# Kernel optimization log

Hardware: AMD Instinct MI355X
Metric: run time of the kernel (lower is better)

The kernel has to match this reference:

```python
import jax, jax.numpy as jnp
import numpy as np

P = 16          # patch size
ER = 2          # expand_ratio = per-head dim in Hgru2

def _shift2d(x, sh, sw):
    # zero-fill shift of (B,C,H,W) image by (sh, sw); matches torch F.pad((l,r,t,b)) with a negative crop
    H, W = x.shape[2], x.shape[3]
    ah, aw = abs(sh), abs(sw)
    xp = jnp.pad(x, ((0, 0), (0, 0), (ah, ah), (aw, aw)))
    return xp[:, :, ah - sh:ah - sh + H, aw - sw:aw - sw + W]

def _layernorm(x, g, b, eps=1e-5):
    m = jnp.mean(x, axis=-1, keepdims=True)
    v = jnp.var(x, axis=-1, keepdims=True)
    return (x - m) * jax.lax.rsqrt(v + eps) * g + b

def _rmsnorm(x, eps=1e-6):
    # FastSimpleRMSNorm: weightless RMS normalization
    return x * jax.lax.rsqrt(jnp.mean(x * x, axis=-1, keepdims=True) + eps)

def _hgru2(x, lb_vec, wi, wo):
    # x: (N, T, D). NOTE: the torch module unpacks x.shape as (n, b, d), so the
    # gated linear recurrence scans over axis 0 exactly as the original does.
    N, T, D = x.shape
    H = D // ER
    feat = x @ wi                                    # (N, T, 3D)
    V, Q, Fg = jnp.split(feat, 3, axis=-1)
    V = jax.nn.gelu(V, approximate=False).reshape(N, T, H, ER)
    Q = jax.nn.gelu(Q, approximate=False).reshape(N, T, H, ER)
    Fg = jax.nn.sigmoid(Fg).reshape(N, T, H, ER)
    lb = lb_vec.reshape(H, ER)
    lam = lb + (1.0 - lb) * Fg                       # decay lambda_t in (lb, 1)
    K = 1.0 - lam
    def step(S, inp):
        q, k, v, l = inp                             # each (T, H, ER)
        # S[t,h,i,j] = lam[i] * S + k[i] * v[j]  (GLA recurrence, 2x2 state/head)
        S = l[..., None] * S + k[..., None] * v[..., None, :]
        o = jnp.einsum('thi,thij->thj', q, S)
        return S, o
    S0 = jnp.zeros((T, H, ER, ER), dtype=x.dtype)
    _, o = jax.lax.scan(step, S0, (Q, K, V, lam))    # o: (N, T, H, ER)
    return o.reshape(N, T, D) @ wo

def reference(img, spt_ln_g, spt_ln_b, spt_w, spt_b, pos_emb, cls_token, lower_bounds,
              in_proj_w, out_proj_w, ff_w1, ff_b1, ff_w2, ff_b2,
              head_ln_g, head_ln_b, head_w, head_b):
    B, C, Hh, Ww = img.shape
    # SPT: concat original + 4 shifted copies on channel axis -> (B, 5C, H, W)
    xs = jnp.concatenate([img,
                          _shift2d(img, 0, 1), _shift2d(img, 0, -1),
                          _shift2d(img, 1, 0), _shift2d(img, -1, 0)], axis=1)
    c5 = 5 * C
    h, w = Hh // P, Ww // P
    # 'b c (h p1) (w p2) -> b (h w) (p1 p2 c)'
    patches = xs.reshape(B, c5, h, P, w, P).transpose(0, 2, 4, 3, 5, 1).reshape(B, h * w, P * P * c5)
    tokens = _layernorm(patches, spt_ln_g, spt_ln_b) @ spt_w + spt_b   # (B, NP, D)
    n = tokens.shape[1]
    cls = jnp.broadcast_to(cls_token, (B, 1, tokens.shape[2]))
    x = jnp.concatenate([cls, tokens], axis=1) + pos_emb[:, :n + 1]
    # layer-wise monotone lower bounds for the decay gate
    lb = jax.nn.softmax(lower_bounds, axis=0)
    lb = jnp.cumsum(lb, axis=0)
    lb = lb - lb[0]
    depth = lower_bounds.shape[0]
    for i in range(depth):
        x = _hgru2(_rmsnorm(x), lb[i], in_proj_w[i], out_proj_w[i]) + x
        hmid = jax.nn.gelu(_rmsnorm(x) @ ff_w1[i] + ff_b1[i], approximate=False)
        x = hmid @ ff_w2[i] + ff_b2[i] + x
    x = _rmsnorm(x)
    x = x[:, 0]                                      # cls pooling
    return _layernorm(x, head_ln_g, head_ln_b) @ head_w + head_b

def setup_inputs():
    key = jax.random.key(0)
    ks = jax.random.split(key, 10)
    B, C, IMG, D, DEPTH, MLP, NC = 16, 3, 256, 768, 8, 3072, 1000
    NP = (IMG // P) ** 2
    PD = P * P * 5 * C
    s = 0.02
    return {
        'img': jax.random.normal(ks[0], (B, C, IMG, IMG), jnp.float32),
        'spt_ln_g': jnp.ones((PD,), jnp.float32),
        'spt_ln_b': jnp.zeros((PD,), jnp.float32),
        'spt_w': jax.random.normal(ks[1], (PD, D), jnp.float32) * s,
        'spt_b': jnp.zeros((D,), jnp.float32),
        'pos_emb': jax.random.normal(ks[2], (1, NP + 1, D), jnp.float32),
        'cls_token': jax.random.normal(ks[3], (1, 1, D), jnp.float32),
        'lower_bounds': jnp.ones((DEPTH, D), jnp.float32),
        'in_proj_w': jax.random.normal(ks[4], (DEPTH, D, 3 * D), jnp.float32) * s,
        'out_proj_w': jax.random.normal(ks[5], (DEPTH, D, D), jnp.float32) * s,
        'ff_w1': jax.random.normal(ks[6], (DEPTH, D, MLP), jnp.float32) * s,
        'ff_b1': jnp.zeros((DEPTH, MLP), jnp.float32),
        'ff_w2': jax.random.normal(ks[7], (DEPTH, MLP, D), jnp.float32) * s,
        'ff_b2': jnp.zeros((DEPTH, D), jnp.float32),
        'head_ln_g': jnp.ones((D,), jnp.float32),
        'head_ln_b': jnp.zeros((D,), jnp.float32),
        'head_w': jax.random.normal(ks[8], (D, NC), jnp.float32) * s,
        'head_b': jnp.zeros((NC,), jnp.float32),
    }
```

## Files before the change

### kernel.cpp

```cpp
#include <hip/hip_runtime.h>
#include <hip/hip_bf16.h>

typedef __bf16 bf16x8 __attribute__((ext_vector_type(8)));
typedef float floatx4 __attribute__((ext_vector_type(4)));

#define DEV __device__ __forceinline__

DEV float gelu_f(float x) {
    return 0.5f * x * (1.0f + erff(x * 0.70710678118654752f));
}

DEV void block_reduce2(float& a, float& b, float* s) {
    #pragma unroll
    for (int o = 32; o > 0; o >>= 1) {
        a += __shfl_down(a, o, 64);
        b += __shfl_down(b, o, 64);
    }
    __syncthreads();
    int wv = threadIdx.x >> 6;
    if ((threadIdx.x & 63) == 0) { s[wv * 2] = a; s[wv * 2 + 1] = b; }
    __syncthreads();
    int nw = blockDim.x >> 6;
    float ra = 0.f, rb = 0.f;
    for (int i = 0; i < nw; ++i) { ra += s[i * 2]; rb += s[i * 2 + 1]; }
    a = ra; b = rb;
}

__global__ __launch_bounds__(256) void compute_lb(const float* __restrict__ lbin, float* __restrict__ lbout) {
    int d = blockIdx.x * 256 + threadIdx.x;
    if (d >= 768) return;
    float v[8];
    float mx = -1e30f;
    #pragma unroll
    for (int i = 0; i < 8; ++i) { v[i] = lbin[i * 768 + d]; mx = fmaxf(mx, v[i]); }
    float s = 0.f;
    #pragma unroll
    for (int i = 0; i < 8; ++i) { v[i] = expf(v[i] - mx); s += v[i]; }
    float inv = 1.f / s;
    float first = v[0] * inv;
    float cum = 0.f;
    #pragma unroll
    for (int i = 0; i < 8; ++i) { cum += v[i] * inv; lbout[i * 768 + d] = cum - first; }
}

__global__ __launch_bounds__(256) void init_tokens(const float* __restrict__ cls, const float* __restrict__ pos,
                                                   const float* __restrict__ bias, float* __restrict__ x) {
    int i = blockIdx.x * 256 + threadIdx.x;
    if (i >= 16 * 257 * 768) return;
    int d = i % 768;
    int row = i / 768;
    int t = row % 257;
    float v;
    if (t == 0) v = cls[d] + pos[d];
    else        v = bias[d] + pos[(size_t)t * 768 + d];
    x[(size_t)row * 768 + d] = v;
}

__global__ __launch_bounds__(256) void patch_ln(const float* __restrict__ img, const float* __restrict__ g,
                                                const float* __restrict__ bt, __hip_bfloat16* __restrict__ out) {
    int pm = blockIdx.x;
    int b = pm >> 8, pp = pm & 255;
    int ph = pp >> 4, pw = pp & 15;
    __shared__ float pv[3840];
    __shared__ float sbuf[8];
    float s = 0.f, ss = 0.f;
    #pragma unroll
    for (int i = 0; i < 15; ++i) {
        int f = threadIdx.x + i * 256;
        int pi = f / 15, cc = f % 15;
        int ip = pi >> 4, jp = pi & 15;
        int g5 = cc / 3, ch = cc % 3;
        int sh = (g5 == 3) - (g5 == 4);
        int sw = (g5 == 1) - (g5 == 2);
        int y = ph * 16 + ip - sh;
        int x = pw * 16 + jp - sw;
        float val = 0.f;
        if ((unsigned)y < 256u && (unsigned)x < 256u)
            val = img[(((size_t)b * 3 + ch) * 256 + y) * 256 + x];
        pv[f] = val; s += val; ss += val * val;
    }
    block_reduce2(s, ss, sbuf);
    float mean = s * (1.f / 3840.f);
    float var  = ss * (1.f / 3840.f) - mean * mean;
    float inv  = rsqrtf(var + 1e-5f);
    #pragma unroll
    for (int i = 0; i < 15; ++i) {
        int f = threadIdx.x + i * 256;
        out[(size_t)pm * 3840 + f] = __float2bfloat16((pv[f] - mean) * inv * g[f] + bt[f]);
    }
}

__global__ __launch_bounds__(256) void transpose_cast(const float* __restrict__ W, __hip_bfloat16* __restrict__ Wt,
                                                      int K, int N) {
    __shared__ float tile[32][33];
    int k0 = blockIdx.x * 32, n0 = blockIdx.y * 32;
    int tx = threadIdx.x & 31, ty = threadIdx.x >> 5;
    #pragma unroll
    for (int i = 0; i < 4; ++i) {
        int k = ty + i * 8;
        tile[k][tx] = W[(size_t)(k0 + k) * N + n0 + tx];
    }
    __syncthreads();
    #pragma unroll
    for (int i = 0; i < 4; ++i) {
        int n = ty + i * 8;
        Wt[(size_t)(n0 + n) * K + k0 + tx] = __float2bfloat16(tile[tx][n]);
    }
}

__global__ __launch_bounds__(256) void rmsnorm_kernel(const float* __restrict__ x, __hip_bfloat16* __restrict__ out) {
    int row = blockIdx.x;
    const float* xr = x + (size_t)row * 768;
    __shared__ float sbuf[8];
    float v[3];
    float ss = 0.f, d0 = 0.f;
    #pragma unroll
    for (int i = 0; i < 3; ++i) { v[i] = xr[threadIdx.x + i * 256]; ss += v[i] * v[i]; }
    block_reduce2(ss, d0, sbuf);
    float scale = rsqrtf(ss * (1.f / 768.f) + 1e-6f);
    #pragma unroll
    for (int i = 0; i < 3; ++i)
        out[(size_t)row * 768 + threadIdx.x + i * 256] = __float2bfloat16(v[i] * scale);
}

__global__ __launch_bounds__(256) void hgru_scan(const float* __restrict__ feat, __hip_bfloat16* __restrict__ o) {
    int idx = blockIdx.x * 256 + threadIdx.x;
    if (idx >= 257 * 384) return;
    int t = idx / 384, h = idx % 384;
    float2 V[16], Q[16], L[16];
    #pragma unroll
    for (int n = 0; n < 16; ++n) {
        size_t base = ((size_t)n * 257 + t) * 2304 + h * 2;
        V[n] = *(const float2*)(feat + base);
        Q[n] = *(const float2*)(feat + base + 768);
        L[n] = *(const float2*)(feat + base + 1536);
    }
    float S00 = 0.f, S01 = 0.f, S10 = 0.f, S11 = 0.f;
    #pragma unroll
    for (int n = 0; n < 16; ++n) {
        float l0 = L[n].x, l1 = L[n].y;
        float k0 = 1.f - l0, k1 = 1.f - l1;
        S00 = l0 * S00 + k0 * V[n].x; S01 = l0 * S01 + k0 * V[n].y;
        S10 = l1 * S10 + k1 * V[n].x; S11 = l1 * S11 + k1 * V[n].y;
        float o0 = Q[n].x * S00 + Q[n].y * S10;
        float o1 = Q[n].x * S01 + Q[n].y * S11;
        __hip_bfloat162 ov;
        ov.x = __float2bfloat16(o0);
        ov.y = __float2bfloat16(o1);
        *(__hip_bfloat162*)(o + ((size_t)n * 257 + t) * 768 + h * 2) = ov;
    }
}

__global__ __launch_bounds__(256) void head_kernel(const float* __restrict__ x, const float* __restrict__ g,
                                                   const float* __restrict__ be, const float* __restrict__ hw,
                                                   const float* __restrict__ hb, float* __restrict__ out) {
    int b = blockIdx.x;
    const float* xr = x + (size_t)b * 257 * 768;
    __shared__ float z[768];
    __shared__ float sbuf[8];
    float v[3];
    float ss = 0.f, d0 = 0.f;
    #pragma unroll
    for (int i = 0; i < 3; ++i) { v[i] = xr[threadIdx.x + i * 256]; ss += v[i] * v[i]; }
    block_reduce2(ss, d0, sbuf);
    float rs = rsqrtf(ss * (1.f / 768.f) + 1e-6f);
    float s = 0.f, s2 = 0.f;
    #pragma unroll
    for (int i = 0; i < 3; ++i) { float y = v[i] * rs; s += y; s2 += y * y; }
    block_reduce2(s, s2, sbuf);
    float mean = s * (1.f / 768.f);
    float var  = s2 * (1.f / 768.f) - mean * mean;
    float inv  = rsqrtf(var + 1e-5f);
    #pragma unroll
    for (int i = 0; i < 3; ++i) {
        int d = threadIdx.x + i * 256;
        z[d] = (v[i] * rs - mean) * inv * g[d] + be[d];
    }
    __syncthreads();
    int j = blockIdx.y * 256 + threadIdx.x;
    if (j < 1000) {
        float acc = hb[j];
        for (int d = 0; d < 768; ++d) acc += z[d] * hw[d * 1000 + j];
        out[b * 1000 + j] = acc;
    }
}

template<int EPI, int BN, int DEPTH>
__global__ __launch_bounds__(256) void gemm_bt(
        const __hip_bfloat16* __restrict__ A, const __hip_bfloat16* __restrict__ Bt,
        int N, int Ktot, int Mvalid,
        float* __restrict__ outf, __hip_bfloat16* __restrict__ outb,
        const float* __restrict__ bias, const float* __restrict__ aux) {
    constexpr int WNF = BN / 32;
    __shared__ alignas(16) __hip_bfloat16 Als[DEPTH][128 * 32];
    __shared__ alignas(16) __hip_bfloat16 Bls[DEPTH][BN * 32];
    const int tid  = threadIdx.x;
    const int lane = tid & 63;
    const int wv   = tid >> 6;

    const int gx = gridDim.x;
    const int nwg = gx * gridDim.y;
    const int orig = blockIdx.x + gx * blockIdx.y;
    const int q = nwg >> 3, r = nwg & 7;
    const int xcd = orig & 7, off = orig >> 3;
    const int wg = (xcd < r ? xcd * (q + 1) : r * (q + 1) + (xcd - r) * q) + off;
    const int n0 = (wg % gx) * BN;
    const int m0 = (wg / gx) * 128;

    const int wm = wv & 1, wn = wv >> 1;
    const int fr = lane & 15;
    const int fq = lane >> 4;
    const int srow = lane >> 2;
    const int ssw  = (((lane & 3) ^ ((srow >> 1) & 3)) * 8);
    const int rsw  = ((fq ^ ((fr >> 1) & 3)) * 8);

    floatx4 acc[4][WNF];
    #pragma unroll
    for (int mi = 0; mi < 4; ++mi)
        #pragma unroll
        for (int ni = 0; ni < WNF; ++ni)
            acc[mi][ni] = (floatx4){0.f, 0.f, 0.f, 0.f};

    auto stage = [&](int kt, int buf) {
        #pragma unroll
        for (int j = 0; j < 2; ++j) {
            int cc = wv * 2 + j;
            const __hip_bfloat16* ga = A + (size_t)(m0 + cc * 16 + srow) * Ktot + kt + ssw;
            __builtin_amdgcn_global_load_lds((const __attribute__((address_space(1))) void*)ga,
                                             (__attribute__((address_space(3))) void*)(&Als[buf][cc * 512]), 16, 0, 0);
        }
        #pragma unroll
        for (int j = 0; j < BN / 64; ++j) {
            int cc = wv * (BN / 64) + j;
            const __hip_bfloat16* gb = Bt + (size_t)(n0 + cc * 16 + srow) * Ktot + kt + ssw;
            __builtin_amdgcn_global_load_lds((const __attribute__((address_space(1))) void*)gb,
                                             (__attribute__((address_space(3))) void*)(&Bls[buf][cc * 512]), 16, 0, 0);
        }
    };

    const int nk = Ktot / 32;
    #pragma unroll
    for (int t = 0; t < DEPTH - 1; ++t) stage(t * 32, t);

    int cur = 0;
    for (int i = 0; i < nk; ++i) {
        if constexpr (DEPTH == 4) {
            if (i + 2 < nk)      asm volatile("s_waitcnt vmcnt(6)" ::: "memory");
            else if (i + 1 < nk) asm volatile("s_waitcnt vmcnt(3)" ::: "memory");
            else                 asm volatile("s_waitcnt vmcnt(0)" ::: "memory");
        } else {
            if (i + 1 < nk) {
                if constexpr (BN == 128) asm volatile("s_waitcnt vmcnt(4)" ::: "memory");
                else                     asm volatile("s_waitcnt vmcnt(3)" ::: "memory");
            } else {
                asm volatile("s_waitcnt vmcnt(0)" ::: "memory");
            }
        }
        __builtin_amdgcn_s_barrier();
        __builtin_amdgcn_sched_barrier(0);

        bf16x8 af[4], bfv[WNF];
        #pragma unroll
        for (int mi = 0; mi < 4; ++mi)
            af[mi] = *(const bf16x8*)((const void*)&Als[cur][(wm * 64 + mi * 16 + fr) * 32 + rsw]);
        #pragma unroll
        for (int ni = 0; ni < WNF; ++ni)
            bfv[ni] = *(const bf16x8*)((const void*)&Bls[cur][(wn * (BN / 2) + ni * 16 + fr) * 32 + rsw]);

        if (i + DEPTH - 1 < nk) stage((i + DEPTH - 1) * 32, cur == 0 ? DEPTH - 1 : cur - 1);

        #pragma unroll
        for (int mi = 0; mi < 4; ++mi)
            #pragma unroll
            for (int ni = 0; ni < WNF; ++ni)
                acc[mi][ni] = __builtin_amdgcn_mfma_f32_16x16x32_bf16(af[mi], bfv[ni], acc[mi][ni], 0, 0, 0);

        cur = (cur == DEPTH - 1) ? 0 : cur + 1;
    }

    const int cr0 = wm * 64 + fq * 4;
    const int cc0 = wn * (BN / 2) + fr;
    #pragma unroll
    for (int mi = 0; mi < 4; ++mi) {
        #pragma unroll
        for (int rr = 0; rr < 4; ++rr) {
            int gm = m0 + cr0 + mi * 16 + rr;
            if (gm >= Mvalid) continue;
            #pragma unroll
            for (int ni = 0; ni < WNF; ++ni) {
                int gn = n0 + cc0 + ni * 16;
                float v = acc[mi][ni][rr];
                if (EPI == 1) {
                    float res;
                    if (gn < 1536) {
                        res = gelu_f(v);
                    } else {
                        float l = aux[gn - 1536];
                        res = l + (1.f - l) / (1.f + expf(-v));
                    }
                    outf[(size_t)gm * N + gn] = res;
                } else if (EPI == 3) {
                    outb[(size_t)gm * N + gn] = __float2bfloat16(gelu_f(v + bias[gn]));
                } else if (EPI == 6) {
                    float add = v + (bias ? bias[gn] : 0.f);
                    outf[(size_t)gm * N + gn] += add;
                } else if (EPI == 7) {
                    size_t orow = (size_t)(gm >> 8) * 257 + 1 + (gm & 255);
                    outf[orow * 768 + gn] += v;
                }
            }
        }
    }
}

extern "C" void kernel_launch(void* const* d_in, const int* in_sizes, int n_in,
                              void* d_out, int out_size, void* d_ws, size_t ws_size,
                              hipStream_t stream) {
    const float* img        = (const float*)d_in[0];
    const float* spt_ln_g   = (const float*)d_in[1];
    const float* spt_ln_b   = (const float*)d_in[2];
    const float* spt_w      = (const float*)d_in[3];
    const float* spt_b      = (const float*)d_in[4];
    const float* pos_emb    = (const float*)d_in[5];
    const float* cls_token  = (const float*)d_in[6];
    const float* lower_bnds = (const float*)d_in[7];
    const float* in_proj_w  = (const float*)d_in[8];
    const float* out_proj_w = (const float*)d_in[9];
    const float* ff_w1      = (const float*)d_in[10];
    const float* ff_b1      = (const float*)d_in[11];
    const float* ff_w2      = (const float*)d_in[12];
    const float* ff_b2      = (const float*)d_in[13];
    const float* head_ln_g  = (const float*)d_in[14];
    const float* head_ln_b  = (const float*)d_in[15];
    const float* head_w     = (const float*)d_in[16];
    const float* head_b     = (const float*)d_in[17];
    float* out = (float*)d_out;

    char* wp = (char*)d_ws;
    auto alloc = [&](size_t bytes) -> void* {
        void* p = (void*)wp;
        wp += (bytes + 255) & ~(size_t)255;
        return p;
    };
    float*          lbbuf   = (float*)         alloc(8 * 768 * 4);
    __hip_bfloat16* patches = (__hip_bfloat16*)alloc((size_t)4096 * 3840 * 2);
    __hip_bfloat16* spt_wt  = (__hip_bfloat16*)alloc((size_t)768 * 3840 * 2);
    float*          xbuf    = (float*)         alloc((size_t)4112 * 768 * 4);
    __hip_bfloat16* normbuf = (__hip_bfloat16*)alloc((size_t)4224 * 768 * 2);
    float*          featbuf = (float*)         alloc((size_t)4112 * 2304 * 4);
    __hip_bfloat16* obuf    = (__hip_bfloat16*)alloc((size_t)4224 * 768 * 2);
    __hip_bfloat16* midbuf  = (__hip_bfloat16*)alloc((size_t)4224 * 3072 * 2);
    __hip_bfloat16* w_in_t  = (__hip_bfloat16*)alloc((size_t)2304 * 768 * 2);
    __hip_bfloat16* w_out_t = (__hip_bfloat16*)alloc((size_t)768 * 768 * 2);
    __hip_bfloat16* w1_t    = (__hip_bfloat16*)alloc((size_t)3072 * 768 * 2);
    __hip_bfloat16* w2_t    = (__hip_bfloat16*)alloc((size_t)768 * 3072 * 2);
    (void)in_sizes; (void)n_in; (void)out_size; (void)ws_size;

    compute_lb<<<3, 256, 0, stream>>>(lower_bnds, lbbuf);
    init_tokens<<<(16 * 257 * 768 + 255) / 256, 256, 0, stream>>>(cls_token, pos_emb, spt_b, xbuf);
    patch_ln<<<4096, 256, 0, stream>>>(img, spt_ln_g, spt_ln_b, patches);
    transpose_cast<<<dim3(3840 / 32, 768 / 32), 256, 0, stream>>>(spt_w, spt_wt, 3840, 768);
    gemm_bt<7, 64, 4><<<dim3(12, 32), 256, 0, stream>>>(patches, spt_wt, 768, 3840, 4096,
                                                        xbuf, nullptr, nullptr, nullptr);

    for (int i = 0; i < 8; ++i) {
        rmsnorm_kernel<<<4112, 256, 0, stream>>>(xbuf, normbuf);
        transpose_cast<<<dim3(24, 72), 256, 0, stream>>>(in_proj_w + (size_t)i * 768 * 2304, w_in_t, 768, 2304);
        gemm_bt<1, 128, 3><<<dim3(18, 33), 256, 0, stream>>>(normbuf, w_in_t, 2304, 768, 4112,
                                                             featbuf, nullptr, nullptr, lbbuf + i * 768);
        hgru_scan<<<386, 256, 0, stream>>>(featbuf, obuf);
        transpose_cast<<<dim3(24, 24), 256, 0, stream>>>(out_proj_w + (size_t)i * 768 * 768, w_out_t, 768, 768);
        gemm_bt<6, 64, 4><<<dim3(12, 33), 256, 0, stream>>>(obuf, w_out_t, 768, 768, 4112,
                                                            xbuf, nullptr, nullptr, nullptr);
        rmsnorm_kernel<<<4112, 256, 0, stream>>>(xbuf, normbuf);
        transpose_cast<<<dim3(24, 96), 256, 0, stream>>>(ff_w1 + (size_t)i * 768 * 3072, w1_t, 768, 3072);
        gemm_bt<3, 128, 3><<<dim3(24, 33), 256, 0, stream>>>(normbuf, w1_t, 3072, 768, 4112,
                                                             nullptr, midbuf, ff_b1 + i * 3072, nullptr);
        transpose_cast<<<dim3(96, 24), 256, 0, stream>>>(ff_w2 + (size_t)i * 3072 * 768, w2_t, 3072, 768);
        gemm_bt<6, 64, 4><<<dim3(12, 33), 256, 0, stream>>>(midbuf, w2_t, 768, 3072, 4112,
                                                            xbuf, nullptr, ff_b2 + i * 768, nullptr);
    }

    head_kernel<<<dim3(16, 4), 256, 0, stream>>>(xbuf, head_ln_g, head_ln_b, head_w, head_b, out);
}
```

Baseline: 1.886 ms.

## Add BK=64 GEMM kernel with XCD-aware tile remap for N=768 projections

Adds a dedicated 128x64-tile GEMM, gemm64, for the N=768 output GEMMs (patch embed, out_proj, FFN down). It stages K in chunks of 64 with triple buffering and an XOR-swizzled LDS layout, and remaps workgroup IDs so neighbouring tiles land on the same XCD. The aim is fewer barriers per K, better L2 locality and fewer LDS bank conflicts. The deeper K tile uses more LDS per block, which may lower occupancy. The DEPTH=4 path is removed from gemm_bt.

```diff
diff --git a/kernel.cpp b/kernel.cpp
--- a/kernel.cpp
+++ b/kernel.cpp
@@ -244,17 +244,11 @@
 
     int cur = 0;
     for (int i = 0; i < nk; ++i) {
-        if constexpr (DEPTH == 4) {
-            if (i + 2 < nk)      asm volatile("s_waitcnt vmcnt(6)" ::: "memory");
-            else if (i + 1 < nk) asm volatile("s_waitcnt vmcnt(3)" ::: "memory");
-            else                 asm volatile("s_waitcnt vmcnt(0)" ::: "memory");
+        if (i + 1 < nk) {
+            if constexpr (BN == 128) asm volatile("s_waitcnt vmcnt(4)" ::: "memory");
+            else                     asm volatile("s_waitcnt vmcnt(3)" ::: "memory");
         } else {
-            if (i + 1 < nk) {
-                if constexpr (BN == 128) asm volatile("s_waitcnt vmcnt(4)" ::: "memory");
-                else                     asm volatile("s_waitcnt vmcnt(3)" ::: "memory");
-            } else {
-                asm volatile("s_waitcnt vmcnt(0)" ::: "memory");
-            }
+            asm volatile("s_waitcnt vmcnt(0)" ::: "memory");
         }
         __builtin_amdgcn_s_barrier();
         __builtin_amdgcn_sched_barrier(0);
@@ -301,7 +295,120 @@
                     outf[(size_t)gm * N + gn] = res;
                 } else if (EPI == 3) {
                     outb[(size_t)gm * N + gn] = __float2bfloat16(gelu_f(v + bias[gn]));
-                } else if (EPI == 6) {
+                }
+            }
+        }
+    }
+}
+
+template<int EPI>
+__global__ __launch_bounds__(256) void gemm64(
+        const __hip_bfloat16* __restrict__ A, const __hip_bfloat16* __restrict__ Bt,
+        int N, int Ktot, int Mvalid,
+        float* __restrict__ outf, const float* __restrict__ bias) {
+    __shared__ alignas(16) __hip_bfloat16 Als[3][128 * 64];
+    __shared__ alignas(16) __hip_bfloat16 Bls[3][64 * 64];
+    const int tid  = threadIdx.x;
+    const int lane = tid & 63;
+    const int wv   = tid >> 6;
+
+    const int gx = gridDim.x;
+    const int nwg = gx * gridDim.y;
+    const int orig = blockIdx.x + gx * blockIdx.y;
+    const int q = nwg >> 3, r = nwg & 7;
+    const int xcd = orig & 7, off = orig >> 3;
+    const int wg = (xcd < r ? xcd * (q + 1) : r * (q + 1) + (xcd - r) * q) + off;
+    const int n0 = (wg % gx) * 64;
+    const int m0 = (wg / gx) * 128;
+
+    const int wm = wv & 1, wn = wv >> 1;
+    const int fr = lane & 15;
+    const int fq = lane >> 4;
+    const int srow8 = lane >> 3;
+    const int slot8 = lane & 7;
+    const int sswz  = (slot8 ^ srow8) * 8;
+
+    floatx4 acc[4][2];
+    #pragma unroll
+    for (int mi = 0; mi < 4; ++mi)
+        #pragma unroll
+        for (int ni = 0; ni < 2; ++ni)
+            acc[mi][ni] = (floatx4){0.f, 0.f, 0.f, 0.f};
+
+    const __hip_bfloat16* pA0 = A  + (size_t)(m0 + wv * 8      + srow8) * Ktot + sswz;
+    const __hip_bfloat16* pA1 = A  + (size_t)(m0 + wv * 8 + 32 + srow8) * Ktot + sswz;
+    const __hip_bfloat16* pA2 = A  + (size_t)(m0 + wv * 8 + 64 + srow8) * Ktot + sswz;
+    const __hip_bfloat16* pA3 = A  + (size_t)(m0 + wv * 8 + 96 + srow8) * Ktot + sswz;
+    const __hip_bfloat16* pB0 = Bt + (size_t)(n0 + wv * 8      + srow8) * Ktot + sswz;
+    const __hip_bfloat16* pB1 = Bt + (size_t)(n0 + wv * 8 + 32 + srow8) * Ktot + sswz;
+
+    auto stage = [&](int kt, int buf) {
+        __hip_bfloat16* la = &Als[buf][(wv * 8) * 64 + lane * 8];
+        __hip_bfloat16* lb = &Bls[buf][(wv * 8) * 64 + lane * 8];
+        __builtin_amdgcn_global_load_lds((const __attribute__((address_space(1))) void*)(pA0 + kt),
+                                         (__attribute__((address_space(3))) void*)(la),            16, 0, 0);
+        __builtin_amdgcn_global_load_lds((const __attribute__((address_space(1))) void*)(pA1 + kt),
+                                         (__attribute__((address_space(3))) void*)(la + 32 * 64),  16, 0, 0);
+        __builtin_amdgcn_global_load_lds((const __attribute__((address_space(1))) void*)(pA2 + kt),
+                                         (__attribute__((address_space(3))) void*)(la + 64 * 64),  16, 0, 0);
+        __builtin_amdgcn_global_load_lds((const __attribute__((address_space(1))) void*)(pA3 + kt),
+                                         (__attribute__((address_space(3))) void*)(la + 96 * 64),  16, 0, 0);
+        __builtin_amdgcn_global_load_lds((const __attribute__((address_space(1))) void*)(pB0 + kt),
+                                         (__attribute__((address_space(3))) void*)(lb),            16, 0, 0);
+        __builtin_amdgcn_global_load_lds((const __attribute__((address_space(1))) void*)(pB1 + kt),
+                                         (__attribute__((address_space(3))) void*)(lb + 32 * 64),  16, 0, 0);
+    };
+
+    const int nk = Ktot / 64;
+    stage(0, 0);
+    stage(64, 1);
+
+    const int rx = fr & 7;
+    int cur = 0;
+    for (int i = 0; i < nk; ++i) {
+        if (i + 1 < nk) asm volatile("s_waitcnt vmcnt(6)" ::: "memory");
+        else            asm volatile("s_waitcnt vmcnt(0)" ::: "memory");
+        __builtin_amdgcn_s_barrier();
+        __builtin_amdgcn_sched_barrier(0);
+
+        bf16x8 af[2][4], bfv[2][2];
+        #pragma unroll
+        for (int s = 0; s < 2; ++s) {
+            int slot = ((s * 4 + fq) ^ rx) * 8;
+            #pragma unroll
+            for (int mi = 0; mi < 4; ++mi)
+                af[s][mi] = *(const bf16x8*)((const void*)&Als[cur][(wm * 64 + mi * 16 + fr) * 64 + slot]);
+            #pragma unroll
+            for (int ni = 0; ni < 2; ++ni)
+                bfv[s][ni] = *(const bf16x8*)((const void*)&Bls[cur][(wn * 32 + ni * 16 + fr) * 64 + slot]);
+        }
+
+        if (i + 2 < nk) stage((i + 2) * 64, cur == 0 ? 2 : cur - 1);
+
+        #pragma unroll
+        for (int s = 0; s < 2; ++s)
+            #pragma unroll
+            for (int mi = 0; mi < 4; ++mi)
+                #pragma unroll
+                for (int ni = 0; ni < 2; ++ni)
+                    acc[mi][ni] = __builtin_amdgcn_mfma_f32_16x16x32_bf16(af[s][mi], bfv[s][ni], acc[mi][ni], 0, 0, 0);
+
+        cur = (cur == 2) ? 0 : cur + 1;
+    }
+
+    const int cr0 = wm * 64 + fq * 4;
+    const int cc0 = wn * 32 + fr;
+    #pragma unroll
+    for (int mi = 0; mi < 4; ++mi) {
+        #pragma unroll
+        for (int rr = 0; rr < 4; ++rr) {
+            int gm = m0 + cr0 + mi * 16 + rr;
+            if (gm >= Mvalid) continue;
+            #pragma unroll
+            for (int ni = 0; ni < 2; ++ni) {
+                int gn = n0 + cc0 + ni * 16;
+                float v = acc[mi][ni][rr];
+                if (EPI == 6) {
                     float add = v + (bias ? bias[gn] : 0.f);
                     outf[(size_t)gm * N + gn] += add;
                 } else if (EPI == 7) {
@@ -360,8 +467,7 @@
     init_tokens<<<(16 * 257 * 768 + 255) / 256, 256, 0, stream>>>(cls_token, pos_emb, spt_b, xbuf);
     patch_ln<<<4096, 256, 0, stream>>>(img, spt_ln_g, spt_ln_b, patches);
     transpose_cast<<<dim3(3840 / 32, 768 / 32), 256, 0, stream>>>(spt_w, spt_wt, 3840, 768);
-    gemm_bt<7, 64, 4><<<dim3(12, 32), 256, 0, stream>>>(patches, spt_wt, 768, 3840, 4096,
-                                                        xbuf, nullptr, nullptr, nullptr);
+    gemm64<7><<<dim3(12, 32), 256, 0, stream>>>(patches, spt_wt, 768, 3840, 4096, xbuf, nullptr);
 
     for (int i = 0; i < 8; ++i) {
         rmsnorm_kernel<<<4112, 256, 0, stream>>>(xbuf, normbuf);
@@ -370,15 +476,13 @@
                                                              featbuf, nullptr, nullptr, lbbuf + i * 768);
         hgru_scan<<<386, 256, 0, stream>>>(featbuf, obuf);
         transpose_cast<<<dim3(24, 24), 256, 0, stream>>>(out_proj_w + (size_t)i * 768 * 768, w_out_t, 768, 768);
-        gemm_bt<6, 64, 4><<<dim3(12, 33), 256, 0, stream>>>(obuf, w_out_t, 768, 768, 4112,
-                                                            xbuf, nullptr, nullptr, nullptr);
+        gemm64<6><<<dim3(12, 33), 256, 0, stream>>>(obuf, w_out_t, 768, 768, 4112, xbuf, nullptr);
         rmsnorm_kernel<<<4112, 256, 0, stream>>>(xbuf, normbuf);
         transpose_cast<<<dim3(24, 96), 256, 0, stream>>>(ff_w1 + (size_t)i * 768 * 3072, w1_t, 768, 3072);
         gemm_bt<3, 128, 3><<<dim3(24, 33), 256, 0, stream>>>(normbuf, w1_t, 3072, 768, 4112,
                                                              nullptr, midbuf, ff_b1 + i * 3072, nullptr);
         transpose_cast<<<dim3(96, 24), 256, 0, stream>>>(ff_w2 + (size_t)i * 3072 * 768, w2_t, 3072, 768);
-        gemm_bt<6, 64, 4><<<dim3(12, 33), 256, 0, stream>>>(midbuf, w2_t, 768, 3072, 4112,
-                                                            xbuf, nullptr, ff_b2 + i * 768, nullptr);
+        gemm64<6><<<dim3(12, 33), 256, 0, stream>>>(midbuf, w2_t, 768, 3072, 4112, xbuf, ff_b2 + i * 768);
     }
 
     head_kernel<<<dim3(16, 4), 256, 0, stream>>>(xbuf, head_ln_g, head_ln_b, head_w, head_b, out);
```

Measured after the change: 1.778 ms. 5.7% less time.
